# Kernel optimization log

Hardware: AMD Instinct MI355X
Metric: run time of the kernel (lower is better)

The kernel has to match this reference:

```python
import jax, jax.numpy as jnp
import numpy as np

E, N, D_IN, HID, TD, H = 800000, 50000, 64, 32, 32, 4
HO = H * HID
VOCAB = 1000000


def time_encode(t, dim):
    # t: [E,1] -> [E,dim], interleaved sin/cos harmonic encoding
    div_term = jnp.exp(jnp.arange(0, dim, 2, dtype=jnp.float32) * (-jnp.log(10000.0) / dim))
    ang = t * div_term  # [E, dim//2]
    return jnp.stack([jnp.sin(ang), jnp.cos(ang)], axis=-1).reshape(t.shape[0], dim)


def tgat_conv(x, src, dst, t_feat, wq, bq, wk, bk, wv, bv, wt, bt, num_nodes):
    # x: [N, Fin]; t_feat: [E, TD]
    q = (x @ wq + bq).reshape(-1, H, HID)
    k = (x @ wk + bk).reshape(-1, H, HID)
    v = (x @ wv + bv).reshape(-1, H, HID)
    te = (t_feat @ wt + bt).reshape(-1, H, HID)
    q_i = q[dst]                      # [E,H,HID] gather at target
    k_j = k[src] + te                 # [E,H,HID] gather at source + time enc
    alpha = jnp.sum(q_i * k_j, axis=-1) / jnp.sqrt(jnp.float32(HID))  # [E,H]
    # segment softmax over edges grouped by destination node
    m = jax.ops.segment_max(alpha, dst, num_segments=num_nodes)        # [N,H]
    ex = jnp.exp(alpha - m[dst])
    s = jax.ops.segment_sum(ex, dst, num_segments=num_nodes)           # [N,H]
    a = ex / (s[dst] + 1e-16)                                          # [E,H]
    msg = v[src] * a[:, :, None]                                       # [E,H,HID]
    out = jax.ops.segment_sum(msg, dst, num_segments=num_nodes)        # [N,H,HID]
    return out.reshape(num_nodes, HO)


def setup_inputs() -> dict:
    key = jax.random.key(0)
    ks = jax.random.split(key, 24)

    def lin_w(k, fi, fo):
        return jax.random.normal(k, (fi, fo), dtype=jnp.float32) / jnp.sqrt(jnp.float32(fi))

    inp = {
        'edge_index': jax.random.randint(ks[0], (2, E), 0, N),
        'edge_attr': jax.random.uniform(ks[1], (E, 2), dtype=jnp.float32),
        'num_nodes': N,
        'emb': jax.random.normal(ks[2], (VOCAB, D_IN), dtype=jnp.float32) * 0.1,
        'wq1': lin_w(ks[3], D_IN, HO), 'bq1': jnp.zeros((HO,), jnp.float32),
        'wk1': lin_w(ks[4], D_IN, HO), 'bk1': jnp.zeros((HO,), jnp.float32),
        'wv1': lin_w(ks[5], D_IN, HO), 'bv1': jnp.zeros((HO,), jnp.float32),
        'wt1': lin_w(ks[6], TD, HO), 'bt1': jnp.zeros((HO,), jnp.float32),
        'wq2': lin_w(ks[7], HO, HO), 'bq2': jnp.zeros((HO,), jnp.float32),
        'wk2': lin_w(ks[8], HO, HO), 'bk2': jnp.zeros((HO,), jnp.float32),
        'wv2': lin_w(ks[9], HO, HO), 'bv2': jnp.zeros((HO,), jnp.float32),
        'wt2': lin_w(ks[10], TD, HO), 'bt2': jnp.zeros((HO,), jnp.float32),
        'wc': lin_w(ks[11], HO, 1), 'bc': jnp.zeros((1,), jnp.float32),
    }
    return inp


def reference(edge_index, edge_attr, num_nodes, emb,
              wq1, bq1, wk1, bk1, wv1, bv1, wt1, bt1,
              wq2, bq2, wk2, bk2, wv2, bv2, wt2, bt2,
              wc, bc):
    src, dst = edge_index[0], edge_index[1]
    x = emb[:num_nodes]                                   # node_emb(arange(N))
    raw_time = edge_attr[:, 1:2]                          # [E,1]
    t_feat = time_encode(raw_time, TD)                    # [E,TD]
    x = jax.nn.relu(tgat_conv(x, src, dst, t_feat, wq1, bq1, wk1, bk1, wv1, bv1, wt1, bt1, num_nodes))
    x = jax.nn.relu(tgat_conv(x, src, dst, t_feat, wq2, bq2, wk2, bk2, wv2, bv2, wt2, bt2, num_nodes))
    edge_emb = x[src] + x[dst]                            # [E,HO]
    return (edge_emb @ wc + bc).squeeze(-1)               # [E]
```

## Files before the change

kernel.cpp:

```cpp
#include <hip/hip_runtime.h>
#include <hip/hip_bf16.h>

#define NNODES 50000
#define HOUT   128
#define NHEAD  4
#define HID    32
#define TDIM   32

typedef _Float16 h8 __attribute__((ext_vector_type(8)));
typedef _Float16 h4 __attribute__((ext_vector_type(4)));
typedef float    f4 __attribute__((ext_vector_type(4)));

__constant__ float DIVT[16] = {
    1.0f, 0.5623413251903491f, 0.31622776601683794f, 0.1778279410038923f,
    0.1f, 0.05623413251903491f, 0.03162277660168379f, 0.01778279410038923f,
    0.01f, 0.005623413251903491f, 0.003162277660168379f, 0.001778279410038923f,
    0.001f, 0.0005623413251903491f, 0.0003162277660168379f, 0.0001778279410038923f
};

__global__ __launch_bounds__(128) void prep_wqt_kernel(
    const float* __restrict__ wq, const float* __restrict__ bq,
    const float* __restrict__ wt, float* __restrict__ wqt,
    float* __restrict__ bqt, int din)
{
    __shared__ float wts[TDIM * HOUT];
    const int tid = threadIdx.x;
    for (int i = tid; i < TDIM * HOUT; i += 128) wts[i] = wt[i];
    __syncthreads();
    const int h = tid >> 5;
    const int t = tid & 31;
    const int d = blockIdx.x;
    const float* row = (d == din) ? bq : wq + (size_t)d * HOUT;
    float s = 0.f;
    #pragma unroll
    for (int d2 = 0; d2 < 32; d2++)
        s += row[h * 32 + d2] * wts[t * HOUT + h * 32 + d2];
    if (d == din) bqt[h * 32 + t] = s;
    else          wqt[(size_t)d * HOUT + h * 32 + t] = s;
}

__global__ void prep_wsplit_kernel(
    const float* __restrict__ W0, const float* __restrict__ W1,
    const float* __restrict__ W2, const float* __restrict__ W3,
    _Float16* __restrict__ hi, _Float16* __restrict__ lo, int din)
{
    const int y = blockIdx.y, col = blockIdx.x, k = threadIdx.x;
    const float* W = (y == 0) ? W0 : (y == 1) ? W1 : (y == 2) ? W2 : W3;
    const float w = W[(size_t)k * HOUT + col];
    const _Float16 h = (_Float16)w;
    const size_t idx = ((size_t)y * HOUT + col) * din + k;
    hi[idx] = h;
    lo[idx] = (_Float16)(w - (float)h);
}

#define GPITCH 72

__global__ __launch_bounds__(256) void gemm_qkv_mfma_kernel(
    const float* __restrict__ X, int din, int n,
    const _Float16* __restrict__ Whi, const _Float16* __restrict__ Wlo,
    const float* __restrict__ B0, const float* __restrict__ B1,
    const float* __restrict__ B2, const float* __restrict__ B3,
    float* __restrict__ q, _Float16* __restrict__ kv, float* __restrict__ qwt)
{
    const int y = blockIdx.y;
    const float* B = (y == 0) ? B0 : (y == 1) ? B1 : (y == 2) ? B2 : B3;
    const _Float16* Wy_hi = Whi + (size_t)y * HOUT * din;
    const _Float16* Wy_lo = Wlo + (size_t)y * HOUT * din;

    __shared__ _Float16 Xh[64 * GPITCH];
    __shared__ _Float16 Xl[64 * GPITCH];
    __shared__ _Float16 Bh[128 * GPITCH];
    __shared__ _Float16 Bl[128 * GPITCH];

    const int tid  = threadIdx.x;
    const int row0 = blockIdx.x * 64;
    const int wv   = tid >> 6;
    const int lane = tid & 63;
    const int lm   = lane & 15;
    const int g    = lane >> 4;

    f4 acc[8];
    #pragma unroll
    for (int ct = 0; ct < 8; ct++) acc[ct] = (f4){0.f, 0.f, 0.f, 0.f};

    float bias[8];
    #pragma unroll
    for (int ct = 0; ct < 8; ct++) bias[ct] = B[ct * 16 + lm];

    const int ktiles = din >> 6;
    for (int kt = 0; kt < ktiles; kt++) {
        {
            const int lrow = tid >> 2;
            const int k0   = (tid & 3) << 4;
            const int grow = row0 + lrow;
            const float* src = X + (size_t)grow * din + kt * 64 + k0;
            #pragma unroll
            for (int i = 0; i < 4; i++) {
                float4 v = (grow < n) ? ((const float4*)src)[i]
                                      : make_float4(0.f, 0.f, 0.f, 0.f);
                h4 hi, lo;
                hi[0] = (_Float16)v.x; hi[1] = (_Float16)v.y;
                hi[2] = (_Float16)v.z; hi[3] = (_Float16)v.w;
                lo[0] = (_Float16)(v.x - (float)hi[0]);
                lo[1] = (_Float16)(v.y - (float)hi[1]);
                lo[2] = (_Float16)(v.z - (float)hi[2]);
                lo[3] = (_Float16)(v.w - (float)hi[3]);
                *(h4*)&Xh[lrow * GPITCH + k0 + 4 * i] = hi;
                *(h4*)&Xl[lrow * GPITCH + k0 + 4 * i] = lo;
            }
        }
        {
            const int col = tid >> 1;
            const int kk0 = (tid & 1) << 5;
            const _Float16* sh = Wy_hi + (size_t)col * din + kt * 64 + kk0;
            const _Float16* sl = Wy_lo + (size_t)col * din + kt * 64 + kk0;
            #pragma unroll
            for (int i = 0; i < 4; i++) {
                *(h8*)&Bh[col * GPITCH + kk0 + 8 * i] = ((const h8*)sh)[i];
                *(h8*)&Bl[col * GPITCH + kk0 + 8 * i] = ((const h8*)sl)[i];
            }
        }
        __syncthreads();

        #pragma unroll
        for (int kc = 0; kc < 2; kc++) {
            const int kb = kc * 32 + g * 8;
            const h8 ah = *(const h8*)&Xh[(wv * 16 + lm) * GPITCH + kb];
            const h8 al = *(const h8*)&Xl[(wv * 16 + lm) * GPITCH + kb];
            #pragma unroll
            for (int ct = 0; ct < 8; ct++) {
                const h8 bh = *(const h8*)&Bh[(ct * 16 + lm) * GPITCH + kb];
                const h8 bl = *(const h8*)&Bl[(ct * 16 + lm) * GPITCH + kb];
                acc[ct] = __builtin_amdgcn_mfma_f32_16x16x32_f16(ah, bh, acc[ct], 0, 0, 0);
                acc[ct] = __builtin_amdgcn_mfma_f32_16x16x32_f16(al, bh, acc[ct], 0, 0, 0);
                acc[ct] = __builtin_amdgcn_mfma_f32_16x16x32_f16(ah, bl, acc[ct], 0, 0, 0);
            }
        }
        __syncthreads();
    }

    #pragma unroll
    for (int ct = 0; ct < 8; ct++) {
        const int col = ct * 16 + lm;
        #pragma unroll
        for (int r = 0; r < 4; r++) {
            const int grow = row0 + wv * 16 + g * 4 + r;
            if (grow >= n) continue;
            const float o = acc[ct][r] + bias[ct];
            if (y == 0)      q[(size_t)grow * HOUT + col] = o;
            else if (y == 3) qwt[(size_t)grow * HOUT + col] = o;
            else             kv[(size_t)grow * 256 + ((y == 1) ? 0 : 128) + col] = (_Float16)o;
        }
    }
}

__global__ __launch_bounds__(256) void hist_kernel(
    const int* __restrict__ ei, int* __restrict__ cnt, int E)
{
    const int e = blockIdx.x * 256 + threadIdx.x;
    if (e >= E) return;
    atomicAdd(&cnt[ei[E + e]], 1);
}

__global__ __launch_bounds__(256) void scan_sum_kernel(
    const int* __restrict__ cnt, int* __restrict__ bsum, int n4)
{
    const int i = blockIdx.x * 256 + threadIdx.x;
    int s = 0;
    if (i < n4) { int4 c = ((const int4*)cnt)[i]; s = c.x + c.y + c.z + c.w; }
    #pragma unroll
    for (int d = 1; d < 64; d <<= 1) s += __shfl_xor(s, d);
    __shared__ int wsum[4];
    if ((threadIdx.x & 63) == 0) wsum[threadIdx.x >> 6] = s;
    __syncthreads();
    if (threadIdx.x == 0) bsum[blockIdx.x] = wsum[0] + wsum[1] + wsum[2] + wsum[3];
}

__global__ __launch_bounds__(64) void scan_top_kernel(
    const int* __restrict__ bsum, int* __restrict__ bpre,
    int* __restrict__ offN, int nb)
{
    const int t = threadIdx.x;
    const int v = (t < nb) ? bsum[t] : 0;
    int incl = v;
    #pragma unroll
    for (int d = 1; d < 64; d <<= 1) {
        int u = __shfl_up(incl, d);
        if (t >= d) incl += u;
    }
    if (t < nb) bpre[t] = incl - v;
    if (t == 63) offN[0] = incl;
}

__global__ __launch_bounds__(256) void scan_write_kernel(
    const int* __restrict__ cnt, const int* __restrict__ bpre,
    int* __restrict__ off, int n4)
{
    const int i = blockIdx.x * 256 + threadIdx.x;
    int4 c = make_int4(0, 0, 0, 0);
    if (i < n4) c = ((const int4*)cnt)[i];
    const int s = c.x + c.y + c.z + c.w;
    int incl = s;
    const int lane = threadIdx.x & 63;
    #pragma unroll
    for (int d = 1; d < 64; d <<= 1) {
        int u = __shfl_up(incl, d);
        if (lane >= d) incl += u;
    }
    __shared__ int wsum[4];
    const int wv = threadIdx.x >> 6;
    if (lane == 63) wsum[wv] = incl;
    __syncthreads();
    int base = bpre[blockIdx.x];
    for (int w = 0; w < wv; w++) base += wsum[w];
    const int excl = base + incl - s;
    if (i < n4)
        ((int4*)off)[i] = make_int4(excl, excl + c.x, excl + c.x + c.y,
                                    excl + c.x + c.y + c.z);
}

__global__ __launch_bounds__(256) void scatter_kernel(
    const int* __restrict__ ei, const float* __restrict__ ea,
    const int* __restrict__ off, int* __restrict__ cur,
    int2* __restrict__ recs, int E)
{
    const int e = blockIdx.x * 256 + threadIdx.x;
    if (e >= E) return;
    const int dn = ei[E + e];
    const int pos = off[dn] + atomicAdd(&cur[dn], 1);
    recs[pos] = make_int2(ei[e], __float_as_int(ea[2 * e + 1]));
}

__global__ __launch_bounds__(256) void node_attn_kernel(
    const int* __restrict__ off, const int2* __restrict__ recs,
    const float* __restrict__ q, const _Float16* __restrict__ kv,
    const float* __restrict__ qwt, const float* __restrict__ bt,
    float* __restrict__ x, const float* __restrict__ wc,
    float* __restrict__ p, int n)
{
    const int wid = (blockIdx.x * 256 + threadIdx.x) >> 6;
    if (wid >= n) return;
    const int lane = threadIdx.x & 63;
    const int slot = lane >> 4;
    const int sub  = lane & 15;
    const int c0   = sub * 8;
    const int dn   = wid;

    const float4* qv = (const float4*)(q   + (size_t)dn * HOUT + c0);
    const float4* wv = (const float4*)(qwt + (size_t)dn * HOUT + c0);
    const float4 q0 = qv[0], q1 = qv[1];
    const float4 w0 = wv[0], w1 = wv[1];

    const float4 bt0 = ((const float4*)(bt + c0))[0];
    const float4 bt1 = ((const float4*)(bt + c0))[1];
    float qb = q0.x * bt0.x + q0.y * bt0.y + q0.z * bt0.z + q0.w * bt0.w +
               q1.x * bt1.x + q1.y * bt1.y + q1.z * bt1.z + q1.w * bt1.w;
    qb += __shfl_xor(qb, 1);
    qb += __shfl_xor(qb, 2);

    const int beg = off[dn];
    const int end = off[dn + 1];

    float acc[8] = {0.f, 0.f, 0.f, 0.f, 0.f, 0.f, 0.f, 0.f};
    float den = 0.f;

    for (int i = beg + slot; i < end; i += 4) {
        const int2 rec = recs[i];
        const int   sn = rec.x;
        const float rt = __int_as_float(rec.y);

        const h8 kk = *(const h8*)(kv + (size_t)sn * 256 + c0);
        const h8 vv = *(const h8*)(kv + (size_t)sn * 256 + 128 + c0);

        const int i0 = (sub & 3) * 4;
        float tf[8];
        #pragma unroll
        for (int jj = 0; jj < 4; jj++) {
            float s_, c_;
            __sincosf(rt * DIVT[i0 + jj], &s_, &c_);
            tf[2 * jj]     = s_;
            tf[2 * jj + 1] = c_;
        }

        float partial =
            q0.x * (float)kk[0] + q0.y * (float)kk[1] +
            q0.z * (float)kk[2] + q0.w * (float)kk[3] +
            q1.x * (float)kk[4] + q1.y * (float)kk[5] +
            q1.z * (float)kk[6] + q1.w * (float)kk[7] +
            w0.x * tf[0] + w0.y * tf[1] + w0.z * tf[2] + w0.w * tf[3] +
            w1.x * tf[4] + w1.y * tf[5] + w1.z * tf[6] + w1.w * tf[7];
        if ((sub & 3) == 0) partial += qb;

        partial += __shfl_xor(partial, 1);
        partial += __shfl_xor(partial, 2);

        const float ex = __expf(partial * 0.17677669529663687f);
        den += ex;
        #pragma unroll
        for (int j = 0; j < 8; j++) acc[j] += ex * (float)vv[j];
    }

    #pragma unroll
    for (int j = 0; j < 8; j++) {
        acc[j] += __shfl_xor(acc[j], 16);
        acc[j] += __shfl_xor(acc[j], 32);
    }
    den += __shfl_xor(den, 16);
    den += __shfl_xor(den, 32);

    if (lane < 16) {
        const float inv = 1.f / (den + 1e-16f);
        float o[8];
        #pragma unroll
        for (int j = 0; j < 8; j++) o[j] = fmaxf(acc[j] * inv, 0.f);
        if (p == nullptr) {
            float* xo = x + (size_t)dn * HOUT + c0;
            *(float4*)xo       = make_float4(o[0], o[1], o[2], o[3]);
            *((float4*)xo + 1) = make_float4(o[4], o[5], o[6], o[7]);
        } else {
            const float4 wc0 = ((const float4*)(wc + c0))[0];
            const float4 wc1 = ((const float4*)(wc + c0))[1];
            float pp = o[0] * wc0.x + o[1] * wc0.y + o[2] * wc0.z + o[3] * wc0.w +
                       o[4] * wc1.x + o[5] * wc1.y + o[6] * wc1.z + o[7] * wc1.w;
            pp += __shfl_xor(pp, 1);
            pp += __shfl_xor(pp, 2);
            pp += __shfl_xor(pp, 4);
            pp += __shfl_xor(pp, 8);
            if (sub == 0) p[dn] = pp;
        }
    }
}

__global__ __launch_bounds__(256) void edge_out_kernel(
    const int* __restrict__ ei, const float* __restrict__ p,
    const float* __restrict__ bc, float* __restrict__ out, int E)
{
    const int e = blockIdx.x * 256 + threadIdx.x;
    if (e >= E) return;
    out[e] = p[ei[e]] + p[ei[E + e]] + bc[0];
}

extern "C" void kernel_launch(void* const* d_in, const int* in_sizes, int n_in,
                              void* d_out, int out_size, void* d_ws, size_t ws_size,
                              hipStream_t stream)
{
    const int E = in_sizes[0] / 2;
    const int N = NNODES;

    const int*   ei  = (const int*)d_in[0];
    const float* ea  = (const float*)d_in[1];
    const float* emb = (const float*)d_in[3];
    const float *wq1 = (const float*)d_in[4],  *bq1 = (const float*)d_in[5];
    const float *wk1 = (const float*)d_in[6],  *bk1 = (const float*)d_in[7];
    const float *wv1 = (const float*)d_in[8],  *bv1 = (const float*)d_in[9];
    const float *wt1 = (const float*)d_in[10], *bt1 = (const float*)d_in[11];
    const float *wq2 = (const float*)d_in[12], *bq2 = (const float*)d_in[13];
    const float *wk2 = (const float*)d_in[14], *bk2 = (const float*)d_in[15];
    const float *wv2 = (const float*)d_in[16], *bv2 = (const float*)d_in[17];
    const float *wt2 = (const float*)d_in[18], *bt2 = (const float*)d_in[19];
    const float *wc  = (const float*)d_in[20], *bc  = (const float*)d_in[21];
    float* out = (float*)d_out;

    float* ws = (float*)d_ws;
    const size_t NF = (size_t)N * HOUT;
    float*     q    = ws;
    float*     qwt  = ws + NF;
    float*     xbuf = ws + 2 * NF;
    _Float16*  kv   = (_Float16*)(ws + 3 * NF);
    int2*      recs = (int2*)(ws + 4 * NF);
    float*     wqt1 = (float*)(recs + E);
    float*     wqt2 = wqt1 + 64 * HOUT;
    float*     bqt1 = wqt2 + 128 * HOUT;
    float*     bqt2 = bqt1 + HOUT;
    _Float16*  whi1 = (_Float16*)(bqt2 + HOUT);
    _Float16*  wlo1 = whi1 + 4 * HOUT * 64;
    _Float16*  whi2 = wlo1 + 4 * HOUT * 64;
    _Float16*  wlo2 = whi2 + 4 * HOUT * 128;
    int*       cnt  = (int*)(wlo2 + 4 * HOUT * 128);
    int*       off  = cnt + N;
    int*       cur  = off + N + 1;
    float*     p    = (float*)(cur + N);
    int*       bsum = (int*)(p + N);
    int*       bpre = bsum + 64;

    const dim3 ggemm((N + 63) / 64, 4);
    const int  eblk  = (E + 255) / 256;
    const int  nblk  = (N + 3) / 4;
    const int  n4    = N / 4;
    const int  sblk  = (n4 + 255) / 256;

    prep_wqt_kernel<<<65, 128, 0, stream>>>(wq1, bq1, wt1, wqt1, bqt1, 64);
    prep_wqt_kernel<<<129, 128, 0, stream>>>(wq2, bq2, wt2, wqt2, bqt2, 128);
    prep_wsplit_kernel<<<dim3(HOUT, 4), 64, 0, stream>>>(wq1, wk1, wv1, wqt1, whi1, wlo1, 64);
    prep_wsplit_kernel<<<dim3(HOUT, 4), 128, 0, stream>>>(wq2, wk2, wv2, wqt2, whi2, wlo2, 128);

    hipMemsetAsync(cnt, 0, (size_t)N * sizeof(int), stream);
    hipMemsetAsync(cur, 0, (size_t)N * sizeof(int), stream);
    hist_kernel<<<eblk, 256, 0, stream>>>(ei, cnt, E);
    scan_sum_kernel<<<sblk, 256, 0, stream>>>(cnt, bsum, n4);
    scan_top_kernel<<<1, 64, 0, stream>>>(bsum, bpre, off + N, sblk);
    scan_write_kernel<<<sblk, 256, 0, stream>>>(cnt, bpre, off, n4);
    scatter_kernel<<<eblk, 256, 0, stream>>>(ei, ea, off, cur, recs, E);

    gemm_qkv_mfma_kernel<<<ggemm, 256, 0, stream>>>(emb, 64, N,
        whi1, wlo1, bq1, bk1, bv1, bqt1, q, kv, qwt);
    node_attn_kernel<<<nblk, 256, 0, stream>>>(off, recs, q, kv, qwt, bt1,
                                               xbuf, nullptr, nullptr, N);

    gemm_qkv_mfma_kernel<<<ggemm, 256, 0, stream>>>(xbuf, 128, N,
        whi2, wlo2, bq2, bk2, bv2, bqt2, q, kv, qwt);
    node_attn_kernel<<<nblk, 256, 0, stream>>>(off, recs, q, kv, qwt, bt2,
                                               nullptr, wc, p, N);

    edge_out_kernel<<<(E + 255) / 256, 256, 0, stream>>>(ei, p, bc, out, E);
}
```

Measured before the change: 656.5 us.

## Software-pipeline edge loads in node attention, fuse prep and scan kernels

The node attention loop now prefetches the next edge record and its K/V rows one iteration ahead, and the record two iterations ahead, so gather latency overlaps the current edge's math. The time encoding uses the hardware sin/cos instructions with divisors prescaled by 1/(2π) instead of __sincosf. The weight-prep kernels are merged into one, which computes Wq·Wt inline, and the scan top-level kernel is folded into scan_write, cutting several launches. In exchange, register pressure rises and the hardware sin/cos may lose accuracy for large arguments.

```diff
diff --git a/kernel.cpp b/kernel.cpp
--- a/kernel.cpp
+++ b/kernel.cpp
@@ -11,46 +11,44 @@
 typedef _Float16 h4 __attribute__((ext_vector_type(4)));
 typedef float    f4 __attribute__((ext_vector_type(4)));
 
-__constant__ float DIVT[16] = {
-    1.0f, 0.5623413251903491f, 0.31622776601683794f, 0.1778279410038923f,
-    0.1f, 0.05623413251903491f, 0.03162277660168379f, 0.01778279410038923f,
-    0.01f, 0.005623413251903491f, 0.003162277660168379f, 0.001778279410038923f,
-    0.001f, 0.0005623413251903491f, 0.0003162277660168379f, 0.0001778279410038923f
+__constant__ float DIVT_REV[16] = {
+    0.15915494309189535f,   0.08950140093327467f,   0.050329212595f,        0.028302204f,
+    0.015915494309189535f,  0.008950140093327467f,  0.0050329212595f,       0.0028302204f,
+    0.0015915494309189535f, 0.0008950140093327467f, 0.00050329212595f,      0.00028302204f,
+    0.00015915494309189535f,0.00008950140093327467f,0.000050329212595f,     0.000028302204f
 };
 
-__global__ __launch_bounds__(128) void prep_wqt_kernel(
-    const float* __restrict__ wq, const float* __restrict__ bq,
-    const float* __restrict__ wt, float* __restrict__ wqt,
+__global__ __launch_bounds__(128) void prep_layer_kernel(
+    const float* __restrict__ wq, const float* __restrict__ wk,
+    const float* __restrict__ wv, const float* __restrict__ wt,
+    const float* __restrict__ bq,
+    _Float16* __restrict__ hi, _Float16* __restrict__ lo,
     float* __restrict__ bqt, int din)
 {
-    __shared__ float wts[TDIM * HOUT];
-    const int tid = threadIdx.x;
-    for (int i = tid; i < TDIM * HOUT; i += 128) wts[i] = wt[i];
-    __syncthreads();
-    const int h = tid >> 5;
-    const int t = tid & 31;
-    const int d = blockIdx.x;
-    const float* row = (d == din) ? bq : wq + (size_t)d * HOUT;
-    float s = 0.f;
-    #pragma unroll
-    for (int d2 = 0; d2 < 32; d2++)
-        s += row[h * 32 + d2] * wts[t * HOUT + h * 32 + d2];
-    if (d == din) bqt[h * 32 + t] = s;
-    else          wqt[(size_t)d * HOUT + h * 32 + t] = s;
-}
-
-__global__ void prep_wsplit_kernel(
-    const float* __restrict__ W0, const float* __restrict__ W1,
-    const float* __restrict__ W2, const float* __restrict__ W3,
-    _Float16* __restrict__ hi, _Float16* __restrict__ lo, int din)
-{
     const int y = blockIdx.y, col = blockIdx.x, k = threadIdx.x;
-    const float* W = (y == 0) ? W0 : (y == 1) ? W1 : (y == 2) ? W2 : W3;
-    const float w = W[(size_t)k * HOUT + col];
-    const _Float16 h = (_Float16)w;
+    float w;
+    if (y < 3) {
+        const float* W = (y == 0) ? wq : (y == 1) ? wk : wv;
+        w = W[(size_t)k * HOUT + col];
+    } else {
+        const int h = col >> 5, t = col & 31;
+        const float* wqr = wq + (size_t)k * HOUT + h * 32;
+        const float* wtr = wt + (size_t)t * HOUT + h * 32;
+        float s = 0.f;
+        #pragma unroll
+        for (int d2 = 0; d2 < 32; d2++) s += wqr[d2] * wtr[d2];
+        w = s;
+        if (k == 0) {
+            float sb = 0.f;
+            #pragma unroll
+            for (int d2 = 0; d2 < 32; d2++) sb += bq[h * 32 + d2] * wtr[d2];
+            bqt[col] = sb;
+        }
+    }
+    const _Float16 h16 = (_Float16)w;
     const size_t idx = ((size_t)y * HOUT + col) * din + k;
-    hi[idx] = h;
-    lo[idx] = (_Float16)(w - (float)h);
+    hi[idx] = h16;
+    lo[idx] = (_Float16)(w - (float)h16);
 }
 
 #define GPITCH 72
@@ -176,47 +174,46 @@
     if (threadIdx.x == 0) bsum[blockIdx.x] = wsum[0] + wsum[1] + wsum[2] + wsum[3];
 }
 
-__global__ __launch_bounds__(64) void scan_top_kernel(
-    const int* __restrict__ bsum, int* __restrict__ bpre,
-    int* __restrict__ offN, int nb)
-{
-    const int t = threadIdx.x;
-    const int v = (t < nb) ? bsum[t] : 0;
-    int incl = v;
-    #pragma unroll
-    for (int d = 1; d < 64; d <<= 1) {
-        int u = __shfl_up(incl, d);
-        if (t >= d) incl += u;
-    }
-    if (t < nb) bpre[t] = incl - v;
-    if (t == 63) offN[0] = incl;
-}
-
 __global__ __launch_bounds__(256) void scan_write_kernel(
-    const int* __restrict__ cnt, const int* __restrict__ bpre,
-    int* __restrict__ off, int n4)
-{
+    const int* __restrict__ cnt, const int* __restrict__ bsum,
+    int* __restrict__ off, int n4, int nb, int E)
+{
+    __shared__ int bpre_s;
+    __shared__ int wsum[4];
+    const int lane = threadIdx.x & 63;
+    if (threadIdx.x < 64) {
+        int v = (lane < nb) ? bsum[lane] : 0;
+        int incl = v;
+        #pragma unroll
+        for (int d = 1; d < 64; d <<= 1) {
+            int u = __shfl_up(incl, d);
+            if (lane >= d) incl += u;
+        }
+        const int pre = (blockIdx.x == 0) ? 0 : __shfl(incl, blockIdx.x - 1);
+        if (threadIdx.x == 0) bpre_s = pre;
+    }
+
     const int i = blockIdx.x * 256 + threadIdx.x;
     int4 c = make_int4(0, 0, 0, 0);
     if (i < n4) c = ((const int4*)cnt)[i];
     const int s = c.x + c.y + c.z + c.w;
     int incl = s;
-    const int lane = threadIdx.x & 63;
     #pragma unroll
     for (int d = 1; d < 64; d <<= 1) {
         int u = __shfl_up(incl, d);
         if (lane >= d) incl += u;
     }
-    __shared__ int wsum[4];
     const int wv = threadIdx.x >> 6;
+    __syncthreads();
     if (lane == 63) wsum[wv] = incl;
     __syncthreads();
-    int base = bpre[blockIdx.x];
+    int base = bpre_s;
     for (int w = 0; w < wv; w++) base += wsum[w];
     const int excl = base + incl - s;
     if (i < n4)
         ((int4*)off)[i] = make_int4(excl, excl + c.x, excl + c.x + c.y,
                                     excl + c.x + c.y + c.z);
+    if (blockIdx.x == 0 && threadIdx.x == 0) off[NNODES] = E;
 }
 
 __global__ __launch_bounds__(256) void scatter_kernel(
@@ -245,6 +242,7 @@
     const int sub  = lane & 15;
     const int c0   = sub * 8;
     const int dn   = wid;
+    const int i0   = (sub & 3) * 4;
 
     const float4* qv = (const float4*)(q   + (size_t)dn * HOUT + c0);
     const float4* wv = (const float4*)(qwt + (size_t)dn * HOUT + c0);
@@ -264,22 +262,35 @@
     float acc[8] = {0.f, 0.f, 0.f, 0.f, 0.f, 0.f, 0.f, 0.f};
     float den = 0.f;
 
-    for (int i = beg + slot; i < end; i += 4) {
-        const int2 rec = recs[i];
-        const int   sn = rec.x;
-        const float rt = __int_as_float(rec.y);
-
-        const h8 kk = *(const h8*)(kv + (size_t)sn * 256 + c0);
-        const h8 vv = *(const h8*)(kv + (size_t)sn * 256 + 128 + c0);
-
-        const int i0 = (sub & 3) * 4;
+    int i = beg + slot;
+    int2 rec0 = make_int2(0, 0), rec1 = make_int2(0, 0);
+    h8 kk = {0, 0, 0, 0, 0, 0, 0, 0};
+    h8 vv = {0, 0, 0, 0, 0, 0, 0, 0};
+    if (i < end)     rec0 = recs[i];
+    if (i + 4 < end) rec1 = recs[i + 4];
+    if (i < end) {
+        const _Float16* kp = kv + (size_t)rec0.x * 256 + c0;
+        kk = *(const h8*)kp;
+        vv = *(const h8*)(kp + 128);
+    }
+
+    while (i < end) {
+        int2 rec2 = make_int2(0, 0);
+        if (i + 8 < end) rec2 = recs[i + 8];
+        h8 kkn = kk, vvn = vv;
+        if (i + 4 < end) {
+            const _Float16* kp = kv + (size_t)rec1.x * 256 + c0;
+            kkn = *(const h8*)kp;
+            vvn = *(const h8*)(kp + 128);
+        }
+
+        const float rt = __int_as_float(rec0.y);
         float tf[8];
         #pragma unroll
         for (int jj = 0; jj < 4; jj++) {
-            float s_, c_;
-            __sincosf(rt * DIVT[i0 + jj], &s_, &c_);
-            tf[2 * jj]     = s_;
-            tf[2 * jj + 1] = c_;
+            const float rev = rt * DIVT_REV[i0 + jj];
+            tf[2 * jj]     = __builtin_amdgcn_sinf(rev);
+            tf[2 * jj + 1] = __builtin_amdgcn_cosf(rev);
         }
 
         float partial =
@@ -298,6 +309,9 @@
         den += ex;
         #pragma unroll
         for (int j = 0; j < 8; j++) acc[j] += ex * (float)vv[j];
+
+        i += 4;
+        rec0 = rec1; rec1 = rec2; kk = kkn; vv = vvn;
     }
 
     #pragma unroll
@@ -368,9 +382,7 @@
     float*     xbuf = ws + 2 * NF;
     _Float16*  kv   = (_Float16*)(ws + 3 * NF);
     int2*      recs = (int2*)(ws + 4 * NF);
-    float*     wqt1 = (float*)(recs + E);
-    float*     wqt2 = wqt1 + 64 * HOUT;
-    float*     bqt1 = wqt2 + 128 * HOUT;
+    float*     bqt1 = (float*)(recs + E);
     float*     bqt2 = bqt1 + HOUT;
     _Float16*  whi1 = (_Float16*)(bqt2 + HOUT);
     _Float16*  wlo1 = whi1 + 4 * HOUT * 64;
@@ -381,7 +393,6 @@
     int*       cur  = off + N + 1;
     float*     p    = (float*)(cur + N);
     int*       bsum = (int*)(p + N);
-    int*       bpre = bsum + 64;
 
     const dim3 ggemm((N + 63) / 64, 4);
     const int  eblk  = (E + 255) / 256;
@@ -389,17 +400,16 @@
     const int  n4    = N / 4;
     const int  sblk  = (n4 + 255) / 256;
 
-    prep_wqt_kernel<<<65, 128, 0, stream>>>(wq1, bq1, wt1, wqt1, bqt1, 64);
-    prep_wqt_kernel<<<129, 128, 0, stream>>>(wq2, bq2, wt2, wqt2, bqt2, 128);
-    prep_wsplit_kernel<<<dim3(HOUT, 4), 64, 0, stream>>>(wq1, wk1, wv1, wqt1, whi1, wlo1, 64);
-    prep_wsplit_kernel<<<dim3(HOUT, 4), 128, 0, stream>>>(wq2, wk2, wv2, wqt2, whi2, wlo2, 128);
+    prep_layer_kernel<<<dim3(HOUT, 4), 64, 0, stream>>>(
+        wq1, wk1, wv1, wt1, bq1, whi1, wlo1, bqt1, 64);
+    prep_layer_kernel<<<dim3(HOUT, 4), 128, 0, stream>>>(
+        wq2, wk2, wv2, wt2, bq2, whi2, wlo2, bqt2, 128);
 
     hipMemsetAsync(cnt, 0, (size_t)N * sizeof(int), stream);
     hipMemsetAsync(cur, 0, (size_t)N * sizeof(int), stream);
     hist_kernel<<<eblk, 256, 0, stream>>>(ei, cnt, E);
     scan_sum_kernel<<<sblk, 256, 0, stream>>>(cnt, bsum, n4);
-    scan_top_kernel<<<1, 64, 0, stream>>>(bsum, bpre, off + N, sblk);
-    scan_write_kernel<<<sblk, 256, 0, stream>>>(cnt, bpre, off, n4);
+    scan_write_kernel<<<sblk, 256, 0, stream>>>(cnt, bsum, off, n4, sblk, E);
     scatter_kernel<<<eblk, 256, 0, stream>>>(ei, ea, off, cur, recs, E);
 
     gemm_qkv_mfma_kernel<<<ggemm, 256, 0, stream>>>(emb, 64, N,
```

Measured after the change: 648.0 us. No clear change (-1.3%).
